# Performance work log

Hardware: AMD Instinct MI355X
Metric: run time of the kernel (lower is better)

## Reference

```python
import jax, jax.numpy as jnp
import numpy as np

NM, ND, E, H, HEADS = 1043, 2166, 512, 512, 8
EMM, EDD = 66752, 138624


def setup_inputs() -> dict:
    ks = iter(jax.random.split(jax.random.key(0), 64))
    def nk():
        return next(ks)
    s = 0.05
    inp = {
        'mirna_x': jax.random.normal(nk(), (NM, E), jnp.float32),
        'drug_x': jax.random.normal(nk(), (ND, E), jnp.float32),
    }
    for name, n, m in [('mm1', NM, EMM), ('mm2', NM, EMM), ('dd1', ND, EDD), ('dd2', ND, EDD)]:
        inp['edge_' + name] = jax.random.randint(nk(), (2, m), 0, n, jnp.int32)
        inp['attr_' + name] = jax.random.uniform(nk(), (m,), jnp.float32)
    for enc in ['m1', 'm2', 'd1', 'd2']:
        inp[enc + '_W1'] = jax.random.normal(nk(), (E, H), jnp.float32) * s
        inp[enc + '_b1'] = jax.random.normal(nk(), (H,), jnp.float32) * s
        inp[enc + '_W2'] = jax.random.normal(nk(), (H, H), jnp.float32) * s
        inp[enc + '_b2'] = jax.random.normal(nk(), (H,), jnp.float32) * s
    for p in ['mir', 'drug']:
        for w in ['Wq', 'Wk', 'Wv', 'Wo']:
            inp[p + '_' + w] = jax.random.normal(nk(), (E, E), jnp.float32) * s
        inp[p + '_fw'] = jax.random.normal(nk(), (4,), jnp.float32) * 0.5
        inp[p + '_fb'] = jax.random.normal(nk(), (1,), jnp.float32) * s
    return inp


def gcn_conv(x, W, b, edge, w):
    # PyG GCNConv: add self-loops (weight 1), symmetric normalization, aggregate at target.
    n = x.shape[0]
    h = x @ W
    loop = jnp.arange(n, dtype=edge.dtype)
    src = jnp.concatenate([edge[0], loop])
    dst = jnp.concatenate([edge[1], loop])
    ww = jnp.concatenate([w, jnp.ones((n,), w.dtype)])
    deg = jax.ops.segment_sum(ww, dst, num_segments=n)
    dis = jnp.where(deg > 0, jax.lax.rsqrt(deg), 0.0)
    norm = dis[src] * ww * dis[dst]  # [E+n]
    out = jax.ops.segment_sum(norm[:, None] * h[src], dst, num_segments=n)
    return out + b


def gcn_encoder(x, edge, w, W1, b1, W2, b2):
    x1 = jax.nn.relu(gcn_conv(x, W1, b1, edge, w))
    x2 = jax.nn.relu(gcn_conv(x1, W2, b2, edge, w))
    return jnp.concatenate([x1, x2], axis=1)  # [N, 2H]


def mha(x, Wq, Wk, Wv, Wo):
    # x: (views=4, N, E); attention over the N (num_features) axis, per view.
    V, N, _ = x.shape
    hd = E // HEADS
    def split(W):
        return (x @ W).reshape(V, N, HEADS, hd).transpose(0, 2, 1, 3)  # (V, h, N, hd)
    q, k, v = split(Wq), split(Wk), split(Wv)
    scores = jnp.einsum('vhnd,vhmd->vhnm', q, k) / jnp.sqrt(jnp.float32(hd))
    a = jax.nn.softmax(scores, axis=-1)
    o = jnp.einsum('vhnm,vhmd->vhnd', a, v).transpose(0, 2, 1, 3).reshape(V, N, E)
    return o @ Wo


def fuse(o, fw, fb):
    # 1x1 Conv2d over 4 channels -> weighted channel sum + bias, then view(E,-1).t()
    y = jnp.einsum('c,cne->ne', fw, o) + fb  # (N, E)
    return y.reshape(E, -1).T  # torch .view(out_channels, -1).t() on row-major data


def view_pipeline(v1, v2, Wq, Wk, Wv, Wo, fw, fb):
    emb = jnp.concatenate([v1, v2], axis=1)  # (N, 4E)
    N = emb.shape[0]
    # torch: .view(1, 4, E, -1) then transpose_(-1, -2) -> (4, N, E) after dropping batch dim
    x = emb.reshape(4, E, N).transpose(0, 2, 1)
    return fuse(mha(x, Wq, Wk, Wv, Wo), fw, fb)


def reference(mirna_x, drug_x, edge_mm1, attr_mm1, edge_mm2, attr_mm2, edge_dd1, attr_dd1, edge_dd2, attr_dd2, m1_W1, m1_b1, m1_W2, m1_b2, m2_W1, m2_b1, m2_W2, m2_b2, d1_W1, d1_b1, d1_W2, d1_b2, d2_W1, d2_b1, d2_W2, d2_b2, mir_Wq, mir_Wk, mir_Wv, mir_Wo, mir_fw, mir_fb, drug_Wq, drug_Wk, drug_Wv, drug_Wo, drug_fw, drug_fb):
    mv1 = gcn_encoder(mirna_x, edge_mm1, attr_mm1, m1_W1, m1_b1, m1_W2, m1_b2)
    mv2 = gcn_encoder(mirna_x, edge_mm2, attr_mm2, m2_W1, m2_b1, m2_W2, m2_b2)
    dv1 = gcn_encoder(drug_x, edge_dd1, attr_dd1, d1_W1, d1_b1, d1_W2, d1_b2)
    dv2 = gcn_encoder(drug_x, edge_dd2, attr_dd2, d2_W1, d2_b1, d2_W2, d2_b2)
    mir = view_pipeline(mv1, mv2, mir_Wq, mir_Wk, mir_Wv, mir_Wo, mir_fw, mir_fb)
    drg = view_pipeline(dv1, dv2, drug_Wq, drug_Wk, drug_Wv, drug_Wo, drug_fw, drug_fb)
    return mir @ drg.T  # (1043, 2166)
```

## Files before the change

kernel.cpp:

```cpp
#include <hip/hip_runtime.h>
#include <cmath>

#define NM 1043
#define ND 2166

static inline int ceil_div(int a, int b) { return (a + b - 1) / b; }

typedef __attribute__((ext_vector_type(8))) short bf16x8;
typedef __attribute__((ext_vector_type(4))) float f32x4;
typedef __attribute__((ext_vector_type(2))) unsigned int u32x2;
typedef __attribute__((ext_vector_type(4))) unsigned int u32x4;

union U8 { u32x4 u; bf16x8 h; };

__device__ inline unsigned int pkbf(float a, float b) {
  unsigned int ua = __float_as_uint(a), ub = __float_as_uint(b);
  ua += 0x7FFFu + ((ua >> 16) & 1);
  ub += 0x7FFFu + ((ub >> 16) & 1);
  return (ub & 0xFFFF0000u) | (ua >> 16);
}

__device__ inline unsigned short bf1(float a) {
  unsigned int ua = __float_as_uint(a);
  ua += 0x7FFFu + ((ua >> 16) & 1);
  return (unsigned short)(ua >> 16);
}

struct PrepW { const float* W[16]; unsigned short* Wt[16]; };

__global__ __launch_bounds__(256) void prep_w(PrepW p) {
  const int z = blockIdx.z;
  const float* __restrict__ W = p.W[z];
  unsigned short* __restrict__ Wt = p.Wt[z];
  const int n0 = blockIdx.x * 64, k0 = blockIdx.y * 64;
  __shared__ float Ws[64][65];
  const int tid = threadIdx.x;
#pragma unroll
  for (int it = 0; it < 16; it++) {
    int i = it * 256 + tid;
    int k = i >> 6, n = i & 63;
    Ws[k][n] = W[(size_t)(k0 + k) * 512 + n0 + n];
  }
  __syncthreads();
#pragma unroll
  for (int it = 0; it < 16; it++) {
    int i = it * 256 + tid;
    int n = i >> 6, k = i & 63;
    Wt[(size_t)(n0 + n) * 512 + k0 + k] = bf1(Ws[k][n]);
  }
}

struct BGemm {
  const float* A[6]; const unsigned short* Bt[6]; float* C[6];
  int M[6]; int lda[6];
};

__global__ __launch_bounds__(256) void gemm_mfma(BGemm g) {
  const int z = blockIdx.z;
  const int M = g.M[z];
  const int bm = blockIdx.y << 7;
  if (bm >= M) return;
  const int bn = blockIdx.x << 7;
  const int lda = g.lda[z];
  const float* __restrict__ A = g.A[z];
  const char* __restrict__ Btб = (const char*)g.Bt[z];
  float* __restrict__ C = g.C[z];

  __shared__ short As_s[128 * 64];
  __shared__ short Bs_s[128 * 64];
  char* asb = (char*)As_s;
  char* bsb = (char*)Bs_s;

  const int tid = threadIdx.x;
  const int lane = tid & 63;
  const int w = tid >> 6;
  const int wm = (w >> 1) << 6, wn = (w & 1) << 6;
  const int fr = lane & 15, kg = lane >> 4;

  f32x4 acc[4][4];
#pragma unroll
  for (int i = 0; i < 4; i++)
#pragma unroll
    for (int j = 0; j < 4; j++) acc[i][j] = (f32x4){0.f, 0.f, 0.f, 0.f};

  for (int kb = 0; kb < 512; kb += 64) {
    __syncthreads();
#pragma unroll
    for (int qi = 0; qi < 4; qi++) {
      int qid = qi * 256 + tid;
      int mm = qid >> 3, qk = qid & 7;
      float4 f0 = {}, f1 = {};
      if (bm + mm < M) {
        const float* ap = A + (size_t)(bm + mm) * lda + kb + qk * 8;
        f0 = ((const float4*)ap)[0];
        f1 = ((const float4*)ap)[1];
      }
      u32x4 wv;
      wv.x = pkbf(f0.x, f0.y); wv.y = pkbf(f0.z, f0.w);
      wv.z = pkbf(f1.x, f1.y); wv.w = pkbf(f1.z, f1.w);
      *(u32x4*)(asb + mm * 128 + ((qk * 16) ^ ((mm & 7) << 4))) = wv;
    }
#pragma unroll
    for (int qi = 0; qi < 4; qi++) {
      int qid = qi * 256 + tid;
      int nn = qid >> 3, qk = qid & 7;
      u32x4 bv = *(const u32x4*)(Btб + (((size_t)(bn + nn)) << 10) + (kb + qk * 8) * 2);
      *(u32x4*)(bsb + nn * 128 + ((qk * 16) ^ ((nn & 7) << 4))) = bv;
    }
    __syncthreads();

#pragma unroll
    for (int ks = 0; ks < 2; ks++) {
      bf16x8 af[4], bfv[4];
#pragma unroll
      for (int i = 0; i < 4; i++) {
        int row = wm + i * 16 + fr;
        af[i] = *(const bf16x8*)(asb + row * 128 + (((ks * 64) + kg * 16) ^ ((row & 7) << 4)));
      }
#pragma unroll
      for (int j = 0; j < 4; j++) {
        int row = wn + j * 16 + fr;
        bfv[j] = *(const bf16x8*)(bsb + row * 128 + (((ks * 64) + kg * 16) ^ ((row & 7) << 4)));
      }
#pragma unroll
      for (int i = 0; i < 4; i++)
#pragma unroll
        for (int j = 0; j < 4; j++)
          acc[i][j] = __builtin_amdgcn_mfma_f32_16x16x32_bf16(af[i], bfv[j], acc[i][j], 0, 0, 0);
    }
  }

#pragma unroll
  for (int i = 0; i < 4; i++) {
    int m0 = bm + wm + i * 16 + kg * 4;
#pragma unroll
    for (int j = 0; j < 4; j++) {
      int n = bn + wn + j * 16 + fr;
#pragma unroll
      for (int r = 0; r < 4; r++) {
        if (m0 + r < M) C[(size_t)(m0 + r) * 512 + n] = acc[i][j][r];
      }
    }
  }
}

__global__ __launch_bounds__(256) void gemm_tn(
    const float* __restrict__ A, const float* __restrict__ B, float* __restrict__ C,
    int M, int N, int K, int lda, int ldb, int ldc) {
  __shared__ float As[16][65];
  __shared__ float Bs[16][65];
  const int tid = threadIdx.x;
  const int tx = tid & 15, ty = tid >> 4;
  const int bm = blockIdx.y << 6, bn = blockIdx.x << 6;
  float acc[4][4] = {};
  for (int k0 = 0; k0 < K; k0 += 16) {
    for (int i = tid; i < 16 * 64; i += 256) {
      int kk = i >> 6, mm = i & 63;
      int r = k0 + kk, c = bm + mm;
      As[kk][mm] = (r < K && c < M) ? A[(size_t)r * lda + c] : 0.f;
    }
    for (int i = tid; i < 16 * 64; i += 256) {
      int kk = i >> 6, nn = i & 63;
      int r = k0 + kk, c = bn + nn;
      Bs[kk][nn] = (r < K && c < N) ? B[(size_t)r * ldb + c] : 0.f;
    }
    __syncthreads();
#pragma unroll
    for (int kk = 0; kk < 16; kk++) {
      float a[4], b[4];
#pragma unroll
      for (int i = 0; i < 4; i++) a[i] = As[kk][ty + (i << 4)];
#pragma unroll
      for (int j = 0; j < 4; j++) b[j] = Bs[kk][tx + (j << 4)];
#pragma unroll
      for (int i = 0; i < 4; i++)
#pragma unroll
        for (int j = 0; j < 4; j++) acc[i][j] += a[i] * b[j];
    }
    __syncthreads();
  }
#pragma unroll
  for (int i = 0; i < 4; i++) {
    int r = bm + ty + (i << 4);
    if (r >= M) continue;
#pragma unroll
    for (int j = 0; j < 4; j++) {
      int c = bn + tx + (j << 4);
      if (c < N) C[(size_t)r * ldc + c] = acc[i][j];
    }
  }
}

struct DegB {
  const int* dst[4]; const float* attr[4];
  float* dis[4]; int* cnt[4];
  int epref[5];
};

__global__ __launch_bounds__(256) void deg_count_b(DegB g) {
  int et = blockIdx.x * 256 + threadIdx.x;
  if (et >= g.epref[4]) return;
  int z = (et >= g.epref[1]) + (et >= g.epref[2]) + (et >= g.epref[3]);
  int e = et - g.epref[z];
  int d = g.dst[z][e];
  atomicAdd(&g.dis[z][d], g.attr[z][e]);
  atomicAdd(&g.cnt[z][d], 1);
}

struct FinB { float* dis[4]; int n[4]; };

__global__ __launch_bounds__(256) void finish_dis_b(FinB g) {
  int z = blockIdx.z;
  int i = blockIdx.x * 256 + threadIdx.x;
  if (i < g.n[z]) g.dis[z][i] = rsqrtf(g.dis[z][i] + 1.0f);
}

struct ScanB { const int* cnt[4]; int* rowptr[4]; int n[4]; };

__global__ __launch_bounds__(256) void scan_b(ScanB s) {
  int z = blockIdx.x;
  int n = s.n[z];
  const int* cnt = s.cnt[z];
  int* rp = s.rowptr[z];
  __shared__ int sums[256];
  int tid = threadIdx.x;
  int chunk = (n + 255) >> 8;
  int start = tid * chunk;
  int local = 0;
  for (int i = 0; i < chunk; i++) {
    int idx = start + i;
    if (idx < n) local += cnt[idx];
  }
  sums[tid] = local;
  __syncthreads();
  for (int off = 1; off < 256; off <<= 1) {
    int t = (tid >= off) ? sums[tid - off] : 0;
    __syncthreads();
    sums[tid] += t;
    __syncthreads();
  }
  int base = sums[tid] - local;
  int total = sums[255];
  int run = base;
  for (int i = 0; i < chunk; i++) {
    int idx = start + i;
    if (idx < n) { rp[idx] = run; run += cnt[idx]; }
  }
  if (tid == 0) rp[n] = total;
}

struct FillB {
  const int* src[4]; const int* dst[4]; const float* attr[4];
  const int* rowptr[4]; int* cur[4]; int* col[4]; float* val[4];
  int epref[5];
};

__global__ __launch_bounds__(256) void fill_b(FillB f) {
  int et = blockIdx.x * 256 + threadIdx.x;
  if (et >= f.epref[4]) return;
  int z = (et >= f.epref[1]) + (et >= f.epref[2]) + (et >= f.epref[3]);
  int e = et - f.epref[z];
  int d = f.dst[z][e];
  int pos = f.rowptr[z][d] + atomicAdd(&f.cur[z][d], 1);
  f.col[z][pos] = f.src[z][e];
  f.val[z][pos] = f.attr[z][e];
}

struct GathB {
  const int* rowptr[4]; const int* col[4]; const float* val[4];
  const float* dis[4]; const float* h[4]; const float* b[4];
  float* out[4]; int n[4];
};

__global__ __launch_bounds__(256) void gcn_gather_b(GathB c) {
  const int z = blockIdx.z;
  const int node = blockIdx.x;
  if (node >= c.n[z]) return;
  const int tid = threadIdx.x;
  const int* __restrict__ col = c.col[z];
  const float* __restrict__ val = c.val[z];
  const float* __restrict__ dis = c.dis[z];
  const float* __restrict__ h = c.h[z];
  const int beg = c.rowptr[z][node], end = c.rowptr[z][node + 1];
  float acc0 = 0.f, acc1 = 0.f;
  int e = beg;
  for (; e + 4 <= end; e += 4) {
    int s0 = col[e], s1 = col[e + 1], s2 = col[e + 2], s3 = col[e + 3];
    float w0 = val[e] * dis[s0];
    float w1 = val[e + 1] * dis[s1];
    float w2 = val[e + 2] * dis[s2];
    float w3 = val[e + 3] * dis[s3];
    const float* p0 = h + ((size_t)s0 << 9);
    const float* p1 = h + ((size_t)s1 << 9);
    const float* p2 = h + ((size_t)s2 << 9);
    const float* p3 = h + ((size_t)s3 << 9);
    acc0 += w0 * p0[tid] + w1 * p1[tid] + w2 * p2[tid] + w3 * p3[tid];
    acc1 += w0 * p0[tid + 256] + w1 * p1[tid + 256] + w2 * p2[tid + 256] + w3 * p3[tid + 256];
  }
  for (; e < end; e++) {
    int s = col[e];
    float w = val[e] * dis[s];
    const float* p = h + ((size_t)s << 9);
    acc0 += w * p[tid];
    acc1 += w * p[tid + 256];
  }
  const float dd = dis[node];
  const float* hp = h + ((size_t)node << 9);
  float o0 = fmaxf(dd * acc0 + dd * dd * hp[tid] + c.b[z][tid], 0.f);
  float o1 = fmaxf(dd * acc1 + dd * dd * hp[tid + 256] + c.b[z][tid + 256], 0.f);
  float* op = c.out[z] + (size_t)node * 2048;
  op[tid] = o0;
  op[tid + 256] = o1;
}

struct GatherB { const float* emb[2]; float* xv[2]; int n[2]; };

__global__ __launch_bounds__(256) void gather_b(GatherB g) {
  int z = blockIdx.z;
  int n = g.n[z];
  size_t i = (size_t)blockIdx.x * 256 + threadIdx.x;
  if (i >= (size_t)n * 2048) return;
  int e = (int)(i & 511);
  size_t t = i >> 9;
  int v = (int)(t / n);
  int nn = (int)(t - (size_t)v * n);
  g.xv[z][i] = g.emb[z][((size_t)v * 512 + e) * n + nn];
}

struct AttArgs { const float* Q[2]; const float* K[2]; const float* V[2]; float* O[2]; int N[2]; };

__global__ __launch_bounds__(256) void attn3_kernel(AttArgs ar) {
  const int z = blockIdx.z;
  const int N = ar.N[z];
  const int qb = blockIdx.x * 64;
  if (qb >= N) return;
  const int vh = blockIdx.y, v = vh >> 3, h = vh & 7;
  const size_t base = (size_t)v * N * 512 + (size_t)h * 64;
  const float* __restrict__ Qb = ar.Q[z] + base;
  const float* __restrict__ Kb = ar.K[z] + base;
  const float* __restrict__ Vb = ar.V[z] + base;
  float* __restrict__ Ob = ar.O[z] + base;

  __shared__ short kt_s[64 * 64];
  __shared__ short vt_s[64 * 64];
  char* ktb = (char*)kt_s;
  char* vtb = (char*)vt_s;

  const int tid = threadIdx.x;
  const int lane = tid & 63;
  const int w = tid >> 6;
  const int a15 = lane & 15;
  const int g = lane >> 4;
  const int skr = tid & 63, sg = tid >> 6;
  const int vsr = tid & 15, vsc = tid >> 4;

  const int q = qb + w * 16 + a15;
  bf16x8 qf0, qf1;
  {
    float4 f0 = {}, f1 = {}, f2 = {}, f3 = {};
    if (q < N) {
      const float* qp = Qb + (size_t)q * 512 + g * 8;
      f0 = ((const float4*)qp)[0];
      f1 = ((const float4*)qp)[1];
      f2 = ((const float4*)(qp + 32))[0];
      f3 = ((const float4*)(qp + 32))[1];
    }
    const float s = 0.125f;
    U8 u0, u1;
    u0.u.x = pkbf(f0.x * s, f0.y * s); u0.u.y = pkbf(f0.z * s, f0.w * s);
    u0.u.z = pkbf(f1.x * s, f1.y * s); u0.u.w = pkbf(f1.z * s, f1.w * s);
    u1.u.x = pkbf(f2.x * s, f2.y * s); u1.u.y = pkbf(f2.z * s, f2.w * s);
    u1.u.z = pkbf(f3.x * s, f3.y * s); u1.u.w = pkbf(f3.z * s, f3.w * s);
    qf0 = u0.h; qf1 = u1.h;
  }

  float rm = -INFINITY, rs = 0.f;
  f32x4 o0 = {0.f, 0.f, 0.f, 0.f}, o1 = o0, o2 = o0, o3 = o0;

  const int swzk = (a15 & 7) << 4;
  const int swzv = a15 << 3;

  for (int kb = 0; kb < N; kb += 64) {
    __syncthreads();
    {
      const int row = kb + skr;
      float4 a = {}, b = {}, c = {}, d = {};
      if (row < N) {
        const float* kp = Kb + (size_t)row * 512 + sg * 16;
        a = ((const float4*)kp)[0]; b = ((const float4*)kp)[1];
        c = ((const float4*)kp)[2]; d = ((const float4*)kp)[3];
      }
      const int sw = (skr & 7) << 4;
      u32x4 wk;
      wk.x = pkbf(a.x, a.y); wk.y = pkbf(a.z, a.w);
      wk.z = pkbf(b.x, b.y); wk.w = pkbf(b.z, b.w);
      *(u32x4*)(ktb + skr * 128 + ((sg * 32) ^ sw)) = wk;
      wk.x = pkbf(c.x, c.y); wk.y = pkbf(c.z, c.w);
      wk.z = pkbf(d.x, d.y); wk.w = pkbf(d.z, d.w);
      *(u32x4*)(ktb + skr * 128 + ((sg * 32 + 16) ^ sw)) = wk;
    }
    {
      const int r0 = kb + 4 * vsr;
      float4 f0 = {}, f1 = {}, f2 = {}, f3 = {};
      const float* vp = Vb + (size_t)r0 * 512 + 4 * vsc;
      if (r0 + 0 < N) f0 = *(const float4*)(vp);
      if (r0 + 1 < N) f1 = *(const float4*)(vp + 512);
      if (r0 + 2 < N) f2 = *(const float4*)(vp + 1024);
      if (r0 + 3 < N) f3 = *(const float4*)(vp + 1536);
      const int dd = 4 * vsc;
      const int kby = 8 * vsr;
      u32x2 wv;
      wv.x = pkbf(f0.x, f1.x); wv.y = pkbf(f2.x, f3.x);
      *(u32x2*)(vtb + (dd + 0) * 128 + (kby ^ (((dd + 0) & 15) << 3))) = wv;
      wv.x = pkbf(f0.y, f1.y); wv.y = pkbf(f2.y, f3.y);
      *(u32x2*)(vtb + (dd + 1) * 128 + (kby ^ (((dd + 1) & 15) << 3))) = wv;
      wv.x = pkbf(f0.z, f1.z); wv.y = pkbf(f2.z, f3.z);
      *(u32x2*)(vtb + (dd + 2) * 128 + (kby ^ (((dd + 2) & 15) << 3))) = wv;
      wv.x = pkbf(f0.w, f1.w); wv.y = pkbf(f2.w, f3.w);
      *(u32x2*)(vtb + (dd + 3) * 128 + (kby ^ (((dd + 3) & 15) << 3))) = wv;
    }
    __syncthreads();

    f32x4 sf0 = {0.f, 0.f, 0.f, 0.f}, sf1 = sf0, sf2 = sf0, sf3 = sf0;
#define QK(m, sfm, s2, qfr) \
    sfm = __builtin_amdgcn_mfma_f32_16x16x32_bf16( \
        *(const bf16x8*)(ktb + (16 * m + a15) * 128 + ((64 * s2 + 16 * g) ^ swzk)), \
        qfr, sfm, 0, 0, 0);
    QK(0, sf0, 0, qf0) QK(1, sf1, 0, qf0) QK(2, sf2, 0, qf0) QK(3, sf3, 0, qf0)
    QK(0, sf0, 1, qf1) QK(1, sf1, 1, qf1) QK(2, sf2, 1, qf1) QK(3, sf3, 1, qf1)
#undef QK

    if (kb + 64 > N) {
#define MSK(sfm, m) { int kk = kb + 16 * m + 4 * g; \
      if (kk + 0 >= N) sfm.x = -INFINITY; \
      if (kk + 1 >= N) sfm.y = -INFINITY; \
      if (kk + 2 >= N) sfm.z = -INFINITY; \
      if (kk + 3 >= N) sfm.w = -INFINITY; }
      MSK(sf0, 0) MSK(sf1, 1) MSK(sf2, 2) MSK(sf3, 3)
#undef MSK
    }

    float tmax = fmaxf(fmaxf(fmaxf(sf0.x, sf0.y), fmaxf(sf0.z, sf0.w)),
                       fmaxf(fmaxf(sf1.x, sf1.y), fmaxf(sf1.z, sf1.w)));
    tmax = fmaxf(tmax, fmaxf(fmaxf(fmaxf(sf2.x, sf2.y), fmaxf(sf2.z, sf2.w)),
                             fmaxf(fmaxf(sf3.x, sf3.y), fmaxf(sf3.z, sf3.w))));
    tmax = fmaxf(tmax, __shfl_xor(tmax, 16));
    tmax = fmaxf(tmax, __shfl_xor(tmax, 32));
    const float nm = fmaxf(rm, tmax);
    const float sc = __expf(rm - nm);
    float ps = 0.f;
    u32x4 pr0, pr1, pr2, pr3;
#define SMX(sfm, prm) { float e; unsigned int u; \
    e = __expf(sfm.x - nm); u = __float_as_uint(e); u += 0x7FFFu + ((u >> 16) & 1); u &= 0xFFFF0000u; ps += __uint_as_float(u); prm.x = u; \
    e = __expf(sfm.y - nm); u = __float_as_uint(e); u += 0x7FFFu + ((u >> 16) & 1); u &= 0xFFFF0000u; ps += __uint_as_float(u); prm.y = u; \
    e = __expf(sfm.z - nm); u = __float_as_uint(e); u += 0x7FFFu + ((u >> 16) & 1); u &= 0xFFFF0000u; ps += __uint_as_float(u); prm.z = u; \
    e = __expf(sfm.w - nm); u = __float_as_uint(e); u += 0x7FFFu + ((u >> 16) & 1); u &= 0xFFFF0000u; ps += __uint_as_float(u); prm.w = u; }
    SMX(sf0, pr0) SMX(sf1, pr1) SMX(sf2, pr2) SMX(sf3, pr3)
#undef SMX
    ps += __shfl_xor(ps, 16);
    ps += __shfl_xor(ps, 32);
    rs = rs * sc + ps;
    rm = nm;
    o0 *= sc; o1 *= sc; o2 *= sc; o3 *= sc;

    U8 pb0, pb1;
    pb0.u.x = (pr0.x >> 16) | pr0.y;  pb0.u.y = (pr0.z >> 16) | pr0.w;
    pb0.u.z = (pr1.x >> 16) | pr1.y;  pb0.u.w = (pr1.z >> 16) | pr1.w;
    pb1.u.x = (pr2.x >> 16) | pr2.y;  pb1.u.y = (pr2.z >> 16) | pr2.w;
    pb1.u.z = (pr3.x >> 16) | pr3.y;  pb1.u.w = (pr3.z >> 16) | pr3.w;
#define PV(md, om, s2, pbr) { \
    const char* vr = vtb + (16 * md + a15) * 128; \
    u32x2 v0 = *(const u32x2*)(vr + ((64 * s2 + 8 * g) ^ swzv)); \
    u32x2 v1 = *(const u32x2*)(vr + ((64 * s2 + 32 + 8 * g) ^ swzv)); \
    U8 av; av.u.x = v0.x; av.u.y = v0.y; av.u.z = v1.x; av.u.w = v1.y; \
    om = __builtin_amdgcn_mfma_f32_16x16x32_bf16(av.h, pbr, om, 0, 0, 0); }
    PV(0, o0, 0, pb0.h) PV(1, o1, 0, pb0.h) PV(2, o2, 0, pb0.h) PV(3, o3, 0, pb0.h)
    PV(0, o0, 1, pb1.h) PV(1, o1, 1, pb1.h) PV(2, o2, 1, pb1.h) PV(3, o3, 1, pb1.h)
#undef PV
  }

  if (q < N) {
    const float inv = 1.0f / rs;
    float* op = Ob + (size_t)q * 512 + 4 * g;
    float4 r;
    r.x = o0.x * inv; r.y = o0.y * inv; r.z = o0.z * inv; r.w = o0.w * inv;
    *(float4*)(op + 0) = r;
    r.x = o1.x * inv; r.y = o1.y * inv; r.z = o1.z * inv; r.w = o1.w * inv;
    *(float4*)(op + 16) = r;
    r.x = o2.x * inv; r.y = o2.y * inv; r.z = o2.z * inv; r.w = o2.w * inv;
    *(float4*)(op + 32) = r;
    r.x = o3.x * inv; r.y = o3.y * inv; r.z = o3.z * inv; r.w = o3.w * inv;
    *(float4*)(op + 48) = r;
  }
}

struct FuseB { const float* mha[2]; const float* fw[2]; const float* fb[2]; float* y[2]; int n[2]; };

__global__ __launch_bounds__(256) void fuse_b(FuseB fz) {
  int z = blockIdx.z;
  int n = fz.n[z];
  int i = blockIdx.x * 256 + threadIdx.x;
  if (i >= n * 512) return;
  size_t stride = (size_t)n * 512;
  const float* m = fz.mha[z];
  const float* fw = fz.fw[z];
  float acc = fz.fb[z][0];
  acc += fw[0] * m[i];
  acc += fw[1] * m[stride + i];
  acc += fw[2] * m[2 * stride + i];
  acc += fw[3] * m[3 * stride + i];
  fz.y[z][i] = acc;
}

extern "C" void kernel_launch(void* const* d_in, const int* in_sizes, int n_in,
                              void* d_out, int out_size, void* d_ws, size_t ws_size,
                              hipStream_t stream) {
  const float* mirna_x = (const float*)d_in[0];
  const float* drug_x  = (const float*)d_in[1];
  const int* edge[4] = { (const int*)d_in[2], (const int*)d_in[4], (const int*)d_in[6], (const int*)d_in[8] };
  const float* attr[4] = { (const float*)d_in[3], (const float*)d_in[5], (const float*)d_in[7], (const float*)d_in[9] };
  const int m[4] = { in_sizes[2] / 2, in_sizes[4] / 2, in_sizes[6] / 2, in_sizes[8] / 2 };
  const int nn4[4] = { NM, NM, ND, ND };
  float* out = (float*)d_out;

  float* ws = (float*)d_ws;
  size_t off = 0;
  auto take = [&](size_t nelem) {
    float* r = ws + off;
    off += (nelem + 255) & ~(size_t)255;
    return r;
  };
  const size_t HN = (size_t)NM * 512, HD = (size_t)ND * 512;
  const size_t HALL = 2 * HN + 2 * HD;
  float* emb_m = take((size_t)NM * 2048);
  float* emb_d = take((size_t)ND * 2048);
  float* region = take(2 * HALL);
  float* h4[4] = { region, region + HN, region + 2 * HN, region + 2 * HN + HD };
  float* xv_m = region;
  float* xv_d = region + (size_t)NM * 2048;
  float* dis_all = take(4 * 2560);
  float* dis4[4] = { dis_all, dis_all + 2560, dis_all + 2 * 2560, dis_all + 3 * 2560 };
  int* cnt_all = (int*)take(4 * 2560);
  int* cnt4[4] = { cnt_all, cnt_all + 2560, cnt_all + 2 * 2560, cnt_all + 3 * 2560 };
  int* rp_all = (int*)take(4 * 2304);
  int* rp4[4] = { rp_all, rp_all + 2304, rp_all + 2 * 2304, rp_all + 3 * 2304 };
  int* col4[4];
  float* val4[4];
  for (int z = 0; z < 4; z++) {
    col4[z] = (int*)take(m[z]);
    val4[z] = take(m[z]);
  }
  float* Qm = take((size_t)NM * 2048);
  float* Km = take((size_t)NM * 2048);
  float* Vm = take((size_t)NM * 2048);
  float* Qd = take((size_t)ND * 2048);
  float* Kd = take((size_t)ND * 2048);
  float* Vd = take((size_t)ND * 2048);
  float* y_m = take(HN);
  float* y_d = take(HD);
  unsigned short* wt = (unsigned short*)take((size_t)16 * 131072);

  int pref = 0;
  int epref[5];
  for (int z = 0; z < 4; z++) { epref[z] = pref; pref += m[z]; }
  epref[4] = pref;

  PrepW pw;
  for (int z = 0; z < 4; z++) {
    pw.W[z] = (const float*)d_in[10 + 4 * z];
    pw.W[4 + z] = (const float*)d_in[12 + 4 * z];
    pw.W[8 + z] = (const float*)d_in[26 + z];
    pw.W[12 + z] = (const float*)d_in[32 + z];
  }
  for (int z = 0; z < 16; z++) pw.Wt[z] = wt + (size_t)z * 262144;
  prep_w<<<dim3(8, 8, 16), 256, 0, stream>>>(pw);

  hipMemsetAsync(dis_all, 0, 4 * 2560 * sizeof(float), stream);
  hipMemsetAsync(cnt_all, 0, 4 * 2560 * sizeof(int), stream);

  DegB db;
  for (int z = 0; z < 4; z++) {
    db.dst[z] = edge[z] + m[z]; db.attr[z] = attr[z];
    db.dis[z] = dis4[z]; db.cnt[z] = cnt4[z];
  }
  for (int z = 0; z < 5; z++) db.epref[z] = epref[z];
  deg_count_b<<<ceil_div(pref, 256), 256, 0, stream>>>(db);

  FinB fn;
  for (int z = 0; z < 4; z++) { fn.dis[z] = dis4[z]; fn.n[z] = nn4[z]; }
  finish_dis_b<<<dim3(ceil_div(ND, 256), 1, 4), 256, 0, stream>>>(fn);

  ScanB sb;
  for (int z = 0; z < 4; z++) { sb.cnt[z] = cnt4[z]; sb.rowptr[z] = rp4[z]; sb.n[z] = nn4[z]; }
  scan_b<<<4, 256, 0, stream>>>(sb);

  hipMemsetAsync(cnt_all, 0, 4 * 2560 * sizeof(int), stream);
  FillB fl;
  for (int z = 0; z < 4; z++) {
    fl.src[z] = edge[z]; fl.dst[z] = edge[z] + m[z]; fl.attr[z] = attr[z];
    fl.rowptr[z] = rp4[z]; fl.cur[z] = cnt4[z]; fl.col[z] = col4[z]; fl.val[z] = val4[z];
  }
  for (int z = 0; z < 5; z++) fl.epref[z] = epref[z];
  fill_b<<<ceil_div(pref, 256), 256, 0, stream>>>(fl);

  BGemm c1;
  const float* xin[4] = { mirna_x, mirna_x, drug_x, drug_x };
  for (int z = 0; z < 4; z++) {
    c1.A[z] = xin[z]; c1.Bt[z] = wt + (size_t)z * 262144; c1.C[z] = h4[z];
    c1.M[z] = nn4[z]; c1.lda[z] = 512;
  }
  for (int z = 4; z < 6; z++) { c1.A[z] = nullptr; c1.Bt[z] = nullptr; c1.C[z] = nullptr; c1.M[z] = 0; c1.lda[z] = 512; }
  gemm_mfma<<<dim3(4, ceil_div(ND, 128), 4), 256, 0, stream>>>(c1);

  float* embp[4] = { emb_m, emb_m + 1024, emb_d, emb_d + 1024 };
  GathB g1;
  for (int z = 0; z < 4; z++) {
    g1.rowptr[z] = rp4[z]; g1.col[z] = col4[z]; g1.val[z] = val4[z];
    g1.dis[z] = dis4[z]; g1.h[z] = h4[z]; g1.b[z] = (const float*)d_in[11 + 4 * z];
    g1.out[z] = embp[z]; g1.n[z] = nn4[z];
  }
  gcn_gather_b<<<dim3(ND, 1, 4), 256, 0, stream>>>(g1);

  BGemm c2 = c1;
  for (int z = 0; z < 4; z++) {
    c2.A[z] = embp[z]; c2.Bt[z] = wt + (size_t)(4 + z) * 262144; c2.C[z] = h4[z];
    c2.M[z] = nn4[z]; c2.lda[z] = 2048;
  }
  gemm_mfma<<<dim3(4, ceil_div(ND, 128), 4), 256, 0, stream>>>(c2);

  GathB g2 = g1;
  for (int z = 0; z < 4; z++) { g2.b[z] = (const float*)d_in[13 + 4 * z]; g2.out[z] = embp[z] + 512; }
  gcn_gather_b<<<dim3(ND, 1, 4), 256, 0, stream>>>(g2);

  GatherB gt;
  gt.emb[0] = emb_m; gt.emb[1] = emb_d; gt.xv[0] = xv_m; gt.xv[1] = xv_d;
  gt.n[0] = NM; gt.n[1] = ND;
  gather_b<<<dim3(ceil_div(ND * 2048, 256), 1, 2), 256, 0, stream>>>(gt);

  BGemm qkv;
  float* qkvc[6] = { Qm, Km, Vm, Qd, Kd, Vd };
  for (int z = 0; z < 6; z++) {
    qkv.A[z] = (z < 3) ? xv_m : xv_d;
    qkv.Bt[z] = wt + (size_t)((z < 3) ? (8 + z) : (12 + z - 3)) * 262144;
    qkv.C[z] = qkvc[z];
    qkv.M[z] = (z < 3) ? 4 * NM : 4 * ND; qkv.lda[z] = 512;
  }
  gemm_mfma<<<dim3(4, ceil_div(4 * ND, 128), 6), 256, 0, stream>>>(qkv);

  AttArgs aa;
  aa.Q[0] = Qm; aa.K[0] = Km; aa.V[0] = Vm; aa.O[0] = xv_m; aa.N[0] = NM;
  aa.Q[1] = Qd; aa.K[1] = Kd; aa.V[1] = Vd; aa.O[1] = xv_d; aa.N[1] = ND;
  attn3_kernel<<<dim3(ceil_div(ND, 64), 32, 2), 256, 0, stream>>>(aa);

  BGemm wo;
  for (int z = 0; z < 2; z++) {
    wo.A[z] = (z == 0) ? xv_m : xv_d;
    wo.Bt[z] = wt + (size_t)(z == 0 ? 11 : 15) * 262144;
    wo.C[z] = (z == 0) ? Qm : Qd;
    wo.M[z] = (z == 0) ? 4 * NM : 4 * ND; wo.lda[z] = 512;
  }
  for (int z = 2; z < 6; z++) { wo.A[z] = nullptr; wo.Bt[z] = nullptr; wo.C[z] = nullptr; wo.M[z] = 0; wo.lda[z] = 512; }
  gemm_mfma<<<dim3(4, ceil_div(4 * ND, 128), 2), 256, 0, stream>>>(wo);

  FuseB fz;
  fz.mha[0] = Qm; fz.mha[1] = Qd;
  fz.fw[0] = (const float*)d_in[30]; fz.fw[1] = (const float*)d_in[36];
  fz.fb[0] = (const float*)d_in[31]; fz.fb[1] = (const float*)d_in[37];
  fz.y[0] = y_m; fz.y[1] = y_d;
  fz.n[0] = NM; fz.n[1] = ND;
  fuse_b<<<dim3(ceil_div(ND * 512, 256), 1, 2), 256, 0, stream>>>(fz);

  gemm_tn<<<dim3(ceil_div(ND, 64), ceil_div(NM, 64)), 256, 0, stream>>>(
      y_m, y_d, out, NM, ND, 512, NM, ND, ND);
}
```

Before: 866.5 us.

## Store QKV and attention output in bf16 and process two query tiles per wave

The QKV projection GEMM now writes bf16 directly, the attention kernel reads bf16 Q/K/V without per-tile conversion, and it writes a bf16 output that the Wo GEMM consumes as bf16 input. The attention kernel now handles 128 queries per block (two 16-row query groups per wave), sharing each K fragment load across two MFMAs and halving K/V staging per query. This cuts global memory traffic and conversion work. The cost is higher register pressure from doubled accumulators and slightly different rounding, since the 1/8 scale is now applied after QK instead of before bf16 rounding of Q.

```diff
diff --git a/kernel.cpp b/kernel.cpp
--- a/kernel.cpp
+++ b/kernel.cpp
@@ -51,10 +51,11 @@
 }
 
 struct BGemm {
-  const float* A[6]; const unsigned short* Bt[6]; float* C[6];
+  const void* A[6]; const unsigned short* Bt[6]; void* C[6];
   int M[6]; int lda[6];
 };
 
+template<int AIN_BF16, int COUT_BF16>
 __global__ __launch_bounds__(256) void gemm_mfma(BGemm g) {
   const int z = blockIdx.z;
   const int M = g.M[z];
@@ -62,9 +63,8 @@
   if (bm >= M) return;
   const int bn = blockIdx.x << 7;
   const int lda = g.lda[z];
-  const float* __restrict__ A = g.A[z];
-  const char* __restrict__ Btб = (const char*)g.Bt[z];
-  float* __restrict__ C = g.C[z];
+  const char* __restrict__ Ab = (const char*)g.A[z];
+  const char* __restrict__ Btb = (const char*)g.Bt[z];
 
   __shared__ short As_s[128 * 64];
   __shared__ short Bs_s[128 * 64];
@@ -89,22 +89,25 @@
     for (int qi = 0; qi < 4; qi++) {
       int qid = qi * 256 + tid;
       int mm = qid >> 3, qk = qid & 7;
-      float4 f0 = {}, f1 = {};
+      u32x4 wv = {0u, 0u, 0u, 0u};
       if (bm + mm < M) {
-        const float* ap = A + (size_t)(bm + mm) * lda + kb + qk * 8;
-        f0 = ((const float4*)ap)[0];
-        f1 = ((const float4*)ap)[1];
+        if (AIN_BF16) {
+          wv = *(const u32x4*)(Ab + ((size_t)(bm + mm) * lda + kb + qk * 8) * 2);
+        } else {
+          const float* ap = (const float*)Ab + (size_t)(bm + mm) * lda + kb + qk * 8;
+          float4 f0 = ((const float4*)ap)[0];
+          float4 f1 = ((const float4*)ap)[1];
+          wv.x = pkbf(f0.x, f0.y); wv.y = pkbf(f0.z, f0.w);
+          wv.z = pkbf(f1.x, f1.y); wv.w = pkbf(f1.z, f1.w);
+        }
       }
-      u32x4 wv;
-      wv.x = pkbf(f0.x, f0.y); wv.y = pkbf(f0.z, f0.w);
-      wv.z = pkbf(f1.x, f1.y); wv.w = pkbf(f1.z, f1.w);
       *(u32x4*)(asb + mm * 128 + ((qk * 16) ^ ((mm & 7) << 4))) = wv;
     }
 #pragma unroll
     for (int qi = 0; qi < 4; qi++) {
       int qid = qi * 256 + tid;
       int nn = qid >> 3, qk = qid & 7;
-      u32x4 bv = *(const u32x4*)(Btб + (((size_t)(bn + nn)) << 10) + (kb + qk * 8) * 2);
+      u32x4 bv = *(const u32x4*)(Btb + (((size_t)(bn + nn)) << 10) + (kb + qk * 8) * 2);
       *(u32x4*)(bsb + nn * 128 + ((qk * 16) ^ ((nn & 7) << 4))) = bv;
     }
     __syncthreads();
@@ -138,7 +141,10 @@
       int n = bn + wn + j * 16 + fr;
 #pragma unroll
       for (int r = 0; r < 4; r++) {
-        if (m0 + r < M) C[(size_t)(m0 + r) * 512 + n] = acc[i][j][r];
+        if (m0 + r < M) {
+          if (COUT_BF16) ((unsigned short*)g.C[z])[(size_t)(m0 + r) * 512 + n] = bf1(acc[i][j][r]);
+          else ((float*)g.C[z])[(size_t)(m0 + r) * 512 + n] = acc[i][j][r];
+        }
       }
     }
   }
@@ -327,19 +333,22 @@
   g.xv[z][i] = g.emb[z][((size_t)v * 512 + e) * n + nn];
 }
 
-struct AttArgs { const float* Q[2]; const float* K[2]; const float* V[2]; float* O[2]; int N[2]; };
-
-__global__ __launch_bounds__(256) void attn3_kernel(AttArgs ar) {
+struct AttArgs {
+  const unsigned short* Q[2]; const unsigned short* K[2]; const unsigned short* V[2];
+  unsigned short* O[2]; int N[2];
+};
+
+__global__ __launch_bounds__(256) void attn4_kernel(AttArgs ar) {
   const int z = blockIdx.z;
   const int N = ar.N[z];
-  const int qb = blockIdx.x * 64;
+  const int qb = blockIdx.x * 128;
   if (qb >= N) return;
   const int vh = blockIdx.y, v = vh >> 3, h = vh & 7;
   const size_t base = (size_t)v * N * 512 + (size_t)h * 64;
-  const float* __restrict__ Qb = ar.Q[z] + base;
-  const float* __restrict__ Kb = ar.K[z] + base;
-  const float* __restrict__ Vb = ar.V[z] + base;
-  float* __restrict__ Ob = ar.O[z] + base;
+  const unsigned short* __restrict__ Qb = ar.Q[z] + base;
+  const char* __restrict__ Kc = (const char*)(ar.K[z] + base);
+  const char* __restrict__ Vc = (const char*)(ar.V[z] + base);
+  unsigned short* __restrict__ Ob = ar.O[z] + base;
 
   __shared__ short kt_s[64 * 64];
   __shared__ short vt_s[64 * 64];
@@ -351,146 +360,156 @@
   const int w = tid >> 6;
   const int a15 = lane & 15;
   const int g = lane >> 4;
-  const int skr = tid & 63, sg = tid >> 6;
-  const int vsr = tid & 15, vsc = tid >> 4;
-
-  const int q = qb + w * 16 + a15;
-  bf16x8 qf0, qf1;
-  {
-    float4 f0 = {}, f1 = {}, f2 = {}, f3 = {};
-    if (q < N) {
-      const float* qp = Qb + (size_t)q * 512 + g * 8;
-      f0 = ((const float4*)qp)[0];
-      f1 = ((const float4*)qp)[1];
-      f2 = ((const float4*)(qp + 32))[0];
-      f3 = ((const float4*)(qp + 32))[1];
-    }
-    const float s = 0.125f;
-    U8 u0, u1;
-    u0.u.x = pkbf(f0.x * s, f0.y * s); u0.u.y = pkbf(f0.z * s, f0.w * s);
-    u0.u.z = pkbf(f1.x * s, f1.y * s); u0.u.w = pkbf(f1.z * s, f1.w * s);
-    u1.u.x = pkbf(f2.x * s, f2.y * s); u1.u.y = pkbf(f2.z * s, f2.w * s);
-    u1.u.z = pkbf(f3.x * s, f3.y * s); u1.u.w = pkbf(f3.z * s, f3.w * s);
-    qf0 = u0.h; qf1 = u1.h;
-  }
-
-  float rm = -INFINITY, rs = 0.f;
-  f32x4 o0 = {0.f, 0.f, 0.f, 0.f}, o1 = o0, o2 = o0, o3 = o0;
+
+  const int qA = qb + w * 32 + a15;
+  const int qB = qA + 16;
+  bf16x8 qfA0 = {}, qfA1 = {}, qfB0 = {}, qfB1 = {};
+  if (qA < N) {
+    qfA0 = *(const bf16x8*)(Qb + (size_t)qA * 512 + g * 8);
+    qfA1 = *(const bf16x8*)(Qb + (size_t)qA * 512 + 32 + g * 8);
+  }
+  if (qB < N) {
+    qfB0 = *(const bf16x8*)(Qb + (size_t)qB * 512 + g * 8);
+    qfB1 = *(const bf16x8*)(Qb + (size_t)qB * 512 + 32 + g * 8);
+  }
+
+  float rmA = -INFINITY, rsA = 0.f, rmB = -INFINITY, rsB = 0.f;
+  f32x4 oA0 = {0.f, 0.f, 0.f, 0.f}, oA1 = oA0, oA2 = oA0, oA3 = oA0;
+  f32x4 oB0 = oA0, oB1 = oA0, oB2 = oA0, oB3 = oA0;
 
   const int swzk = (a15 & 7) << 4;
   const int swzv = a15 << 3;
+  const int skr = tid >> 2, skq = (tid & 3) * 16;
+  const int vsr = tid & 15, vsc = tid >> 4;
 
   for (int kb = 0; kb < N; kb += 64) {
     __syncthreads();
     {
-      const int row = kb + skr;
-      float4 a = {}, b = {}, c = {}, d = {};
-      if (row < N) {
-        const float* kp = Kb + (size_t)row * 512 + sg * 16;
-        a = ((const float4*)kp)[0]; b = ((const float4*)kp)[1];
-        c = ((const float4*)kp)[2]; d = ((const float4*)kp)[3];
+      const int sw = (skr & 7) << 4;
+      const char* kp = Kc + (size_t)(kb + skr) * 1024;
+      u32x4 k0 = {0u,0u,0u,0u}, k1 = {0u,0u,0u,0u};
+      if (kb + skr < N) {
+        k0 = *(const u32x4*)(kp + skq);
+        k1 = *(const u32x4*)(kp + skq + 64);
       }
-      const int sw = (skr & 7) << 4;
-      u32x4 wk;
-      wk.x = pkbf(a.x, a.y); wk.y = pkbf(a.z, a.w);
-      wk.z = pkbf(b.x, b.y); wk.w = pkbf(b.z, b.w);
-      *(u32x4*)(ktb + skr * 128 + ((sg * 32) ^ sw)) = wk;
-      wk.x = pkbf(c.x, c.y); wk.y = pkbf(c.z, c.w);
-      wk.z = pkbf(d.x, d.y); wk.w = pkbf(d.z, d.w);
-      *(u32x4*)(ktb + skr * 128 + ((sg * 32 + 16) ^ sw)) = wk;
+      *(u32x4*)(ktb + skr * 128 + (skq ^ sw)) = k0;
+      *(u32x4*)(ktb + skr * 128 + ((skq + 64) ^ sw)) = k1;
     }
     {
       const int r0 = kb + 4 * vsr;
-      float4 f0 = {}, f1 = {}, f2 = {}, f3 = {};
-      const float* vp = Vb + (size_t)r0 * 512 + 4 * vsc;
-      if (r0 + 0 < N) f0 = *(const float4*)(vp);
-      if (r0 + 1 < N) f1 = *(const float4*)(vp + 512);
-      if (r0 + 2 < N) f2 = *(const float4*)(vp + 1024);
-      if (r0 + 3 < N) f3 = *(const float4*)(vp + 1536);
-      const int dd = 4 * vsc;
-      const int kby = 8 * vsr;
-      u32x2 wv;
-      wv.x = pkbf(f0.x, f1.x); wv.y = pkbf(f2.x, f3.x);
-      *(u32x2*)(vtb + (dd + 0) * 128 + (kby ^ (((dd + 0) & 15) << 3))) = wv;
-      wv.x = pkbf(f0.y, f1.y); wv.y = pkbf(f2.y, f3.y);
-      *(u32x2*)(vtb + (dd + 1) * 128 + (kby ^ (((dd + 1) & 15) << 3))) = wv;
-      wv.x = pkbf(f0.z, f1.z); wv.y = pkbf(f2.z, f3.z);
-      *(u32x2*)(vtb + (dd + 2) * 128 + (kby ^ (((dd + 2) & 15) << 3))) = wv;
-      wv.x = pkbf(f0.w, f1.w); wv.y = pkbf(f2.w, f3.w);
-      *(u32x2*)(vtb + (dd + 3) * 128 + (kby ^ (((dd + 3) & 15) << 3))) = wv;
-    }
-    __syncthreads();
-
-    f32x4 sf0 = {0.f, 0.f, 0.f, 0.f}, sf1 = sf0, sf2 = sf0, sf3 = sf0;
-#define QK(m, sfm, s2, qfr) \
-    sfm = __builtin_amdgcn_mfma_f32_16x16x32_bf16( \
-        *(const bf16x8*)(ktb + (16 * m + a15) * 128 + ((64 * s2 + 16 * g) ^ swzk)), \
-        qfr, sfm, 0, 0, 0);
-    QK(0, sf0, 0, qf0) QK(1, sf1, 0, qf0) QK(2, sf2, 0, qf0) QK(3, sf3, 0, qf0)
-    QK(0, sf0, 1, qf1) QK(1, sf1, 1, qf1) QK(2, sf2, 1, qf1) QK(3, sf3, 1, qf1)
-#undef QK
+      u32x2 i0 = {0u,0u}, i1 = {0u,0u}, i2 = {0u,0u}, i3 = {0u,0u};
+      const char* vp = Vc + (size_t)r0 * 1024 + vsc * 8;
+      if (r0 + 0 < N) i0 = *(const u32x2*)(vp);
+      if (r0 + 1 < N) i1 = *(const u32x2*)(vp + 1024);
+      if (r0 + 2 < N) i2 = *(const u32x2*)(vp + 2048);
+      if (r0 + 3 < N) i3 = *(const u32x2*)(vp + 3072);
+      const int dd = 4 * vsc, kby = 8 * vsr;
+      u32x2 o;
+      o.x = (i0.x & 0xFFFFu) | (i1.x << 16); o.y = (i2.x & 0xFFFFu) | (i3.x << 16);
+      *(u32x2*)(vtb + (dd + 0) * 128 + (kby ^ (((dd + 0) & 15) << 3))) = o;
+      o.x = (i0.x >> 16) | (i1.x & 0xFFFF0000u); o.y = (i2.x >> 16) | (i3.x & 0xFFFF0000u);
+      *(u32x2*)(vtb + (dd + 1) * 128 + (kby ^ (((dd + 1) & 15) << 3))) = o;
+      o.x = (i0.y & 0xFFFFu) | (i1.y << 16); o.y = (i2.y & 0xFFFFu) | (i3.y << 16);
+      *(u32x2*)(vtb + (dd + 2) * 128 + (kby ^ (((dd + 2) & 15) << 3))) = o;
+      o.x = (i0.y >> 16) | (i1.y & 0xFFFF0000u); o.y = (i2.y >> 16) | (i3.y & 0xFFFF0000u);
+      *(u32x2*)(vtb + (dd + 3) * 128 + (kby ^ (((dd + 3) & 15) << 3))) = o;
+    }
+    __syncthreads();
+
+    f32x4 sA0 = {0.f,0.f,0.f,0.f}, sA1 = sA0, sA2 = sA0, sA3 = sA0;
+    f32x4 sB0 = sA0, sB1 = sA0, sB2 = sA0, sB3 = sA0;
+#define QK2(m, sAm, sBm, s2, qfa, qfb) { \
+    bf16x8 kf = *(const bf16x8*)(ktb + (16 * m + a15) * 128 + ((64 * s2 + 16 * g) ^ swzk)); \
+    sAm = __builtin_amdgcn_mfma_f32_16x16x32_bf16(kf, qfa, sAm, 0, 0, 0); \
+    sBm = __builtin_amdgcn_mfma_f32_16x16x32_bf16(kf, qfb, sBm, 0, 0, 0); }
+    QK2(0, sA0, sB0, 0, qfA0, qfB0) QK2(1, sA1, sB1, 0, qfA0, qfB0)
+    QK2(2, sA2, sB2, 0, qfA0, qfB0) QK2(3, sA3, sB3, 0, qfA0, qfB0)
+    QK2(0, sA0, sB0, 1, qfA1, qfB1) QK2(1, sA1, sB1, 1, qfA1, qfB1)
+    QK2(2, sA2, sB2, 1, qfA1, qfB1) QK2(3, sA3, sB3, 1, qfA1, qfB1)
+#undef QK2
+
+    sA0 *= 0.125f; sA1 *= 0.125f; sA2 *= 0.125f; sA3 *= 0.125f;
+    sB0 *= 0.125f; sB1 *= 0.125f; sB2 *= 0.125f; sB3 *= 0.125f;
 
     if (kb + 64 > N) {
-#define MSK(sfm, m) { int kk = kb + 16 * m + 4 * g; \
-      if (kk + 0 >= N) sfm.x = -INFINITY; \
-      if (kk + 1 >= N) sfm.y = -INFINITY; \
-      if (kk + 2 >= N) sfm.z = -INFINITY; \
-      if (kk + 3 >= N) sfm.w = -INFINITY; }
-      MSK(sf0, 0) MSK(sf1, 1) MSK(sf2, 2) MSK(sf3, 3)
+#define MSK(sfm, sgm, m) { int kk = kb + 16 * m + 4 * g; \
+      if (kk + 0 >= N) { sfm.x = -INFINITY; sgm.x = -INFINITY; } \
+      if (kk + 1 >= N) { sfm.y = -INFINITY; sgm.y = -INFINITY; } \
+      if (kk + 2 >= N) { sfm.z = -INFINITY; sgm.z = -INFINITY; } \
+      if (kk + 3 >= N) { sfm.w = -INFINITY; sgm.w = -INFINITY; } }
+      MSK(sA0, sB0, 0) MSK(sA1, sB1, 1) MSK(sA2, sB2, 2) MSK(sA3, sB3, 3)
 #undef MSK
     }
 
-    float tmax = fmaxf(fmaxf(fmaxf(sf0.x, sf0.y), fmaxf(sf0.z, sf0.w)),
-                       fmaxf(fmaxf(sf1.x, sf1.y), fmaxf(sf1.z, sf1.w)));
-    tmax = fmaxf(tmax, fmaxf(fmaxf(fmaxf(sf2.x, sf2.y), fmaxf(sf2.z, sf2.w)),
-                             fmaxf(fmaxf(sf3.x, sf3.y), fmaxf(sf3.z, sf3.w))));
-    tmax = fmaxf(tmax, __shfl_xor(tmax, 16));
-    tmax = fmaxf(tmax, __shfl_xor(tmax, 32));
-    const float nm = fmaxf(rm, tmax);
-    const float sc = __expf(rm - nm);
-    float ps = 0.f;
-    u32x4 pr0, pr1, pr2, pr3;
+#define SOFTMAX_PV(sf0, sf1, sf2, sf3, rm, rs, q0, q1, q2, q3) { \
+    float tmax = fmaxf(fmaxf(fmaxf(sf0.x, sf0.y), fmaxf(sf0.z, sf0.w)), \
+                       fmaxf(fmaxf(sf1.x, sf1.y), fmaxf(sf1.z, sf1.w))); \
+    tmax = fmaxf(tmax, fmaxf(fmaxf(fmaxf(sf2.x, sf2.y), fmaxf(sf2.z, sf2.w)), \
+                             fmaxf(fmaxf(sf3.x, sf3.y), fmaxf(sf3.z, sf3.w)))); \
+    tmax = fmaxf(tmax, __shfl_xor(tmax, 16)); \
+    tmax = fmaxf(tmax, __shfl_xor(tmax, 32)); \
+    const float nm = fmaxf(rm, tmax); \
+    const float sc = __expf(rm - nm); \
+    float ps = 0.f; \
+    u32x4 pr0, pr1, pr2, pr3; \
+    SMX(sf0, pr0) SMX(sf1, pr1) SMX(sf2, pr2) SMX(sf3, pr3) \
+    ps += __shfl_xor(ps, 16); \
+    ps += __shfl_xor(ps, 32); \
+    rs = rs * sc + ps; \
+    rm = nm; \
+    q0 *= sc; q1 *= sc; q2 *= sc; q3 *= sc; \
+    U8 pb0, pb1; \
+    pb0.u.x = (pr0.x >> 16) | pr0.y;  pb0.u.y = (pr0.z >> 16) | pr0.w; \
+    pb0.u.z = (pr1.x >> 16) | pr1.y;  pb0.u.w = (pr1.z >> 16) | pr1.w; \
+    pb1.u.x = (pr2.x >> 16) | pr2.y;  pb1.u.y = (pr2.z >> 16) | pr2.w; \
+    pb1.u.z = (pr3.x >> 16) | pr3.y;  pb1.u.w = (pr3.z >> 16) | pr3.w; \
+    PV(0, q0, 0, pb0.h) PV(1, q1, 0, pb0.h) PV(2, q2, 0, pb0.h) PV(3, q3, 0, pb0.h) \
+    PV(0, q0, 1, pb1.h) PV(1, q1, 1, pb1.h) PV(2, q2, 1, pb1.h) PV(3, q3, 1, pb1.h) }
+
 #define SMX(sfm, prm) { float e; unsigned int u; \
     e = __expf(sfm.x - nm); u = __float_as_uint(e); u += 0x7FFFu + ((u >> 16) & 1); u &= 0xFFFF0000u; ps += __uint_as_float(u); prm.x = u; \
     e = __expf(sfm.y - nm); u = __float_as_uint(e); u += 0x7FFFu + ((u >> 16) & 1); u &= 0xFFFF0000u; ps += __uint_as_float(u); prm.y = u; \
     e = __expf(sfm.z - nm); u = __float_as_uint(e); u += 0x7FFFu + ((u >> 16) & 1); u &= 0xFFFF0000u; ps += __uint_as_float(u); prm.z = u; \
     e = __expf(sfm.w - nm); u = __float_as_uint(e); u += 0x7FFFu + ((u >> 16) & 1); u &= 0xFFFF0000u; ps += __uint_as_float(u); prm.w = u; }
-    SMX(sf0, pr0) SMX(sf1, pr1) SMX(sf2, pr2) SMX(sf3, pr3)
-#undef SMX
-    ps += __shfl_xor(ps, 16);
-    ps += __shfl_xor(ps, 32);
-    rs = rs * sc + ps;
-    rm = nm;
-    o0 *= sc; o1 *= sc; o2 *= sc; o3 *= sc;
-
-    U8 pb0, pb1;
-    pb0.u.x = (pr0.x >> 16) | pr0.y;  pb0.u.y = (pr0.z >> 16) | pr0.w;
-    pb0.u.z = (pr1.x >> 16) | pr1.y;  pb0.u.w = (pr1.z >> 16) | pr1.w;
-    pb1.u.x = (pr2.x >> 16) | pr2.y;  pb1.u.y = (pr2.z >> 16) | pr2.w;
-    pb1.u.z = (pr3.x >> 16) | pr3.y;  pb1.u.w = (pr3.z >> 16) | pr3.w;
 #define PV(md, om, s2, pbr) { \
     const char* vr = vtb + (16 * md + a15) * 128; \
     u32x2 v0 = *(const u32x2*)(vr + ((64 * s2 + 8 * g) ^ swzv)); \
     u32x2 v1 = *(const u32x2*)(vr + ((64 * s2 + 32 + 8 * g) ^ swzv)); \
     U8 av; av.u.x = v0.x; av.u.y = v0.y; av.u.z = v1.x; av.u.w = v1.y; \
     om = __builtin_amdgcn_mfma_f32_16x16x32_bf16(av.h, pbr, om, 0, 0, 0); }
-    PV(0, o0, 0, pb0.h) PV(1, o1, 0, pb0.h) PV(2, o2, 0, pb0.h) PV(3, o3, 0, pb0.h)
-    PV(0, o0, 1, pb1.h) PV(1, o1, 1, pb1.h) PV(2, o2, 1, pb1.h) PV(3, o3, 1, pb1.h)
+
+    SOFTMAX_PV(sA0, sA1, sA2, sA3, rmA, rsA, oA0, oA1, oA2, oA3)
+    SOFTMAX_PV(sB0, sB1, sB2, sB3, rmB, rsB, oB0, oB1, oB2, oB3)
 #undef PV
-  }
-
-  if (q < N) {
-    const float inv = 1.0f / rs;
-    float* op = Ob + (size_t)q * 512 + 4 * g;
-    float4 r;
-    r.x = o0.x * inv; r.y = o0.y * inv; r.z = o0.z * inv; r.w = o0.w * inv;
-    *(float4*)(op + 0) = r;
-    r.x = o1.x * inv; r.y = o1.y * inv; r.z = o1.z * inv; r.w = o1.w * inv;
-    *(float4*)(op + 16) = r;
-    r.x = o2.x * inv; r.y = o2.y * inv; r.z = o2.z * inv; r.w = o2.w * inv;
-    *(float4*)(op + 32) = r;
-    r.x = o3.x * inv; r.y = o3.y * inv; r.z = o3.z * inv; r.w = o3.w * inv;
-    *(float4*)(op + 48) = r;
+#undef SMX
+#undef SOFTMAX_PV
+  }
+
+  if (qA < N) {
+    const float inv = 1.0f / rsA;
+    char* op = (char*)(Ob + (size_t)qA * 512) + g * 8;
+    u32x2 r;
+    r.x = pkbf(oA0.x * inv, oA0.y * inv); r.y = pkbf(oA0.z * inv, oA0.w * inv);
+    *(u32x2*)(op) = r;
+    r.x = pkbf(oA1.x * inv, oA1.y * inv); r.y = pkbf(oA1.z * inv, oA1.w * inv);
+    *(u32x2*)(op + 32) = r;
+    r.x = pkbf(oA2.x * inv, oA2.y * inv); r.y = pkbf(oA2.z * inv, oA2.w * inv);
+    *(u32x2*)(op + 64) = r;
+    r.x = pkbf(oA3.x * inv, oA3.y * inv); r.y = pkbf(oA3.z * inv, oA3.w * inv);
+    *(u32x2*)(op + 96) = r;
+  }
+  if (qB < N) {
+    const float inv = 1.0f / rsB;
+    char* op = (char*)(Ob + (size_t)qB * 512) + g * 8;
+    u32x2 r;
+    r.x = pkbf(oB0.x * inv, oB0.y * inv); r.y = pkbf(oB0.z * inv, oB0.w * inv);
+    *(u32x2*)(op) = r;
+    r.x = pkbf(oB1.x * inv, oB1.y * inv); r.y = pkbf(oB1.z * inv, oB1.w * inv);
+    *(u32x2*)(op + 32) = r;
+    r.x = pkbf(oB2.x * inv, oB2.y * inv); r.y = pkbf(oB2.z * inv, oB2.w * inv);
+    *(u32x2*)(op + 64) = r;
+    r.x = pkbf(oB3.x * inv, oB3.y * inv); r.y = pkbf(oB3.z * inv, oB3.w * inv);
+    *(u32x2*)(op + 96) = r;
   }
 }
 
@@ -550,12 +569,14 @@
     col4[z] = (int*)take(m[z]);
     val4[z] = take(m[z]);
   }
-  float* Qm = take((size_t)NM * 2048);
-  float* Km = take((size_t)NM * 2048);
-  float* Vm = take((size_t)NM * 2048);
-  float* Qd = take((size_t)ND * 2048);
-  float* Kd = take((size_t)ND * 2048);
-  float* Vd = take((size_t)ND * 2048);
+  unsigned short* Qm = (unsigned short*)take((size_t)NM * 2048);
+  unsigned short* Km = (unsigned short*)take((size_t)NM * 2048);
+  unsigned short* Vm = (unsigned short*)take((size_t)NM * 2048);
+  unsigned short* Qd = (unsigned short*)take((size_t)ND * 2048);
+  unsigned short* Kd = (unsigned short*)take((size_t)ND * 2048);
+  unsigned short* Vd = (unsigned short*)take((size_t)ND * 2048);
+  float* mha_m = take((size_t)NM * 2048);
+  float* mha_d = take((size_t)ND * 2048);
   float* y_m = take(HN);
   float* y_d = take(HD);
   unsigned short* wt = (unsigned short*)take((size_t)16 * 131072);
@@ -610,7 +631,7 @@
     c1.M[z] = nn4[z]; c1.lda[z] = 512;
   }
   for (int z = 4; z < 6; z++) { c1.A[z] = nullptr; c1.Bt[z] = nullptr; c1.C[z] = nullptr; c1.M[z] = 0; c1.lda[z] = 512; }
-  gemm_mfma<<<dim3(4, ceil_div(ND, 128), 4), 256, 0, stream>>>(c1);
+  gemm_mfma<0, 0><<<dim3(4, ceil_div(ND, 128), 4), 256, 0, stream>>>(c1);
 
   float* embp[4] = { emb_m, emb_m + 1024, emb_d, emb_d + 1024 };
   GathB g1;
@@ -626,7 +647,7 @@
     c2.A[z] = embp[z]; c2.Bt[z] = wt + (size_t)(4 + z) * 262144; c2.C[z] = h4[z];
     c2.M[z] = nn4[z]; c2.lda[z] = 2048;
   }
-  gemm_mfma<<<dim3(4, ceil_div(ND, 128), 4), 256, 0, stream>>>(c2);
+  gemm_mfma<0, 0><<<dim3(4, ceil_div(ND, 128), 4), 256, 0, stream>>>(c2);
 
   GathB g2 = g1;
   for (int z = 0; z < 4; z++) { g2.b[z] = (const float*)d_in[13 + 4 * z]; g2.out[z] = embp[z] + 512; }
@@ -638,32 +659,32 @@
   gather_b<<<dim3(ceil_div(ND * 2048, 256), 1, 2), 256, 0, stream>>>(gt);
 
   BGemm qkv;
-  float* qkvc[6] = { Qm, Km, Vm, Qd, Kd, Vd };
+  unsigned short* qkvc[6] = { Qm, Km, Vm, Qd, Kd, Vd };
   for (int z = 0; z < 6; z++) {
     qkv.A[z] = (z < 3) ? xv_m : xv_d;
     qkv.Bt[z] = wt + (size_t)((z < 3) ? (8 + z) : (12 + z - 3)) * 262144;
     qkv.C[z] = qkvc[z];
     qkv.M[z] = (z < 3) ? 4 * NM : 4 * ND; qkv.lda[z] = 512;
   }
-  gemm_mfma<<<dim3(4, ceil_div(4 * ND, 128), 6), 256, 0, stream>>>(qkv);
+  gemm_mfma<0, 1><<<dim3(4, ceil_div(4 * ND, 128), 6), 256, 0, stream>>>(qkv);
 
   AttArgs aa;
-  aa.Q[0] = Qm; aa.K[0] = Km; aa.V[0] = Vm; aa.O[0] = xv_m; aa.N[0] = NM;
-  aa.Q[1] = Qd; aa.K[1] = Kd; aa.V[1] = Vd; aa.O[1] = xv_d; aa.N[1] = ND;
-  attn3_kernel<<<dim3(ceil_div(ND, 64), 32, 2), 256, 0, stream>>>(aa);
+  aa.Q[0] = Qm; aa.K[0] = Km; aa.V[0] = Vm; aa.O[0] = (unsigned short*)xv_m; aa.N[0] = NM;
+  aa.Q[1] = Qd; aa.K[1] = Kd; aa.V[1] = Vd; aa.O[1] = (unsigned short*)xv_d; aa.N[1] = ND;
+  attn4_kernel<<<dim3(ceil_div(ND, 128), 32, 2), 256, 0, stream>>>(aa);
 
   BGemm wo;
   for (int z = 0; z < 2; z++) {
     wo.A[z] = (z == 0) ? xv_m : xv_d;
     wo.Bt[z] = wt + (size_t)(z == 0 ? 11 : 15) * 262144;
-    wo.C[z] = (z == 0) ? Qm : Qd;
+    wo.C[z] = (z == 0) ? mha_m : mha_d;
     wo.M[z] = (z == 0) ? 4 * NM : 4 * ND; wo.lda[z] = 512;
   }
   for (int z = 2; z < 6; z++) { wo.A[z] = nullptr; wo.Bt[z] = nullptr; wo.C[z] = nullptr; wo.M[z] = 0; wo.lda[z] = 512; }
-  gemm_mfma<<<dim3(4, ceil_div(4 * ND, 128), 2), 256, 0, stream>>>(wo);
+  gemm_mfma<1, 0><<<dim3(4, ceil_div(4 * ND, 128), 2), 256, 0, stream>>>(wo);
 
   FuseB fz;
-  fz.mha[0] = Qm; fz.mha[1] = Qd;
+  fz.mha[0] = mha_m; fz.mha[1] = mha_d;
   fz.fw[0] = (const float*)d_in[30]; fz.fw[1] = (const float*)d_in[36];
   fz.fb[0] = (const float*)d_in[31]; fz.fb[1] = (const float*)d_in[37];
   fz.y[0] = y_m; fz.y[1] = y_d;
```

Measured after the change: 830.0 us. 1.04x faster.
